# Optimization experiments

Hardware: AMD Instinct MI355X
Metric: run time of the kernel (lower is better)

## Reference

```python
import jax, jax.numpy as jnp
import numpy as np

B, C, H, W = 4, 64, 64, 64
CQ = C // 8

def setup_inputs() -> dict:
    key = jax.random.key(0)
    ks = jax.random.split(key, 8)
    s = 1.0 / np.sqrt(C)
    return {
        "x": jax.random.normal(ks[0], (B, C, H, W), dtype=jnp.float32),
        "Wq": jax.random.normal(ks[1], (CQ, C), dtype=jnp.float32) * s,
        "bq": jax.random.normal(ks[2], (CQ,), dtype=jnp.float32) * 0.01,
        "Wk": jax.random.normal(ks[3], (CQ, C), dtype=jnp.float32) * s,
        "bk": jax.random.normal(ks[4], (CQ,), dtype=jnp.float32) * 0.01,
        "Wv": jax.random.normal(ks[5], (C, C), dtype=jnp.float32) * s,
        "bv": jax.random.normal(ks[6], (C,), dtype=jnp.float32) * 0.01,
        "gamma": jax.random.normal(ks[7], (1,), dtype=jnp.float32) * 0.1,
    }

def reference(x, Wq, bq, Wk, bk, Wv, bv, gamma):
    b, c, h, w = x.shape
    n = h * w
    xf = x.reshape(b, c, n)  # [B, C, N]
    # 1x1 convs are pointwise channel projections
    q = jnp.einsum('oc,bcn->bon', Wq, xf) + bq[None, :, None]  # [B, CQ, N]
    k = jnp.einsum('oc,bcn->bon', Wk, xf) + bk[None, :, None]  # [B, CQ, N]
    v = jnp.einsum('oc,bcn->bon', Wv, xf) + bv[None, :, None]  # [B, C, N]
    energy = jnp.einsum('bcn,bcm->bnm', q, k)                  # [B, N, N]
    attn = jax.nn.softmax(energy, axis=-1)
    out = jnp.einsum('bcm,bnm->bcn', v, attn)                  # [B, C, N]
    out = out.reshape(b, c, h, w)
    return gamma[0] * out + x
```

## Files before the change

kernel.cpp:

```cpp
#include <hip/hip_runtime.h>
#include <hip/hip_bf16.h>


typedef __attribute__((ext_vector_type(8))) short short8;
typedef __attribute__((ext_vector_type(4))) float f32x4;
typedef unsigned short ushort_t;

#define NSEQ 4096
#define LOG2E 1.4426950408889634f

__device__ __forceinline__ unsigned pk_bf16(float lo, float hi) {
  union { __hip_bfloat16 b; unsigned short u; } cl, ch;
  cl.b = __float2bfloat16(lo);
  ch.b = __float2bfloat16(hi);
  return (unsigned)cl.u | ((unsigned)ch.u << 16);
}

__global__ __launch_bounds__(256, 4) void proj_kernel(
    const float* __restrict__ x,
    const float* __restrict__ Wq, const float* __restrict__ bq,
    const float* __restrict__ Wk, const float* __restrict__ bk,
    const float* __restrict__ Wv, const float* __restrict__ bv,
    ushort_t* __restrict__ Qb, ushort_t* __restrict__ Kb,
    ushort_t* __restrict__ Vb)
{
  const int tid  = threadIdx.x;
  const int lane = tid & 63;
  const int w    = __builtin_amdgcn_readfirstlane(tid >> 6);
  const int blk  = blockIdx.x;
  const int quarter = blk & 3;
  const int g    = (blk >> 2) & 63;
  const int b    = blk >> 8;
  const int n    = g * 64 + lane;

  const float* xb = x + (size_t)(b * 64) * NSEQ + n;
  const int co0 = quarter * 16 + w * 4;
  const float* w0 = Wv + (co0 + 0) * 64;
  const float* w1 = Wv + (co0 + 1) * 64;
  const float* w2 = Wv + (co0 + 2) * 64;
  const float* w3 = Wv + (co0 + 3) * 64;
  const int p = quarter * 4 + w;
  const float* wr = (p < 8) ? (Wq + p * 64) : (Wk + (p - 8) * 64);
  float a0 = bv[co0 + 0], a1 = bv[co0 + 1], a2 = bv[co0 + 2], a3 = bv[co0 + 3];
  float aq = (p < 8) ? bq[p] : bk[p - 8];

#pragma unroll
  for (int kc = 0; kc < 64; kc += 8) {
    float xv[8];
#pragma unroll
    for (int i = 0; i < 8; ++i) xv[i] = xb[(size_t)(kc + i) * NSEQ];
#pragma unroll
    for (int i = 0; i < 8; ++i) {
      const float xk = xv[i];
      a0 += w0[kc + i] * xk;
      a1 += w1[kc + i] * xk;
      a2 += w2[kc + i] * xk;
      a3 += w3[kc + i] * xk;
      aq += wr[kc + i] * xk;
    }
  }

  union { __hip_bfloat16 h; ushort_t u; } cv;
  ushort_t* vt = Vb + ((size_t)(b * 128 + (n >> 5)) * 64 + co0) * 32 + (n & 31);
  cv.h = __float2bfloat16(a0); vt[0]  = cv.u;
  cv.h = __float2bfloat16(a1); vt[32] = cv.u;
  cv.h = __float2bfloat16(a2); vt[64] = cv.u;
  cv.h = __float2bfloat16(a3); vt[96] = cv.u;

  ushort_t* qk = ((p < 8) ? Qb : Kb) + ((size_t)(b * NSEQ + n)) * 8 + (p & 7);
  cv.h = __float2bfloat16(aq); *qk = cv.u;
}

__global__ __launch_bounds__(256, 2) void attn_kernel(
    const ushort_t* __restrict__ Qb, const ushort_t* __restrict__ Kb,
    const ushort_t* __restrict__ Vb, const float* __restrict__ x,
    const float* __restrict__ gamma, float* __restrict__ out)
{
  __shared__ unsigned P_lds[2][4][2][256];
  __shared__ float red[4][64][35];

  const int tid  = threadIdx.x;
  const int wave = __builtin_amdgcn_readfirstlane(tid >> 6);
  const int lane = tid & 63;
  const int q16  = lane & 15;
  const int quad = lane >> 4;
  const int blk  = blockIdx.x;
  const int b    = blk >> 7;
  const int n0   = (blk & 127) << 5;
  const int mbase = wave << 10;

  const short8 z8 = {0, 0, 0, 0, 0, 0, 0, 0};
  short8 qfA = *(const short8*)(Qb + ((size_t)(b * NSEQ + n0 + q16)) * 8);
  short8 qfB = *(const short8*)(Qb + ((size_t)(b * NSEQ + n0 + 16 + q16)) * 8);
  if (quad != 0) { qfA = z8; qfB = z8; }

  const char* kbase = (const char*)(Kb + ((size_t)(b * NSEQ + mbase + q16)) * 8);
  const char* vbase = (const char*)(Vb + ((size_t)(b * 128 + (mbase >> 5)) * 64) * 32);
  const int voff = q16 * 64 + quad * 16;

  const int sw    = (q16 ^ (q16 >> 2)) & 3;
  const int row16 = q16 * 16;
  const int d0 = 2 * quad, d2 = 8 + 2 * quad;
  const int w00 = row16 + (((d0 >> 2) ^ sw) << 2) + (d0 & 3);
  const int w01 = row16 + ((((d0 + 1) >> 2) ^ sw) << 2) + ((d0 + 1) & 3);
  const int w10 = row16 + (((d2 >> 2) ^ sw) << 2) + (d2 & 3);
  const int w11 = row16 + ((((d2 + 1) >> 2) ^ sw) << 2) + ((d2 + 1) & 3);
  const int rdo = row16 + ((quad ^ sw) << 2);

  f32x4 aA0 = {0.f, 0.f, 0.f, 0.f};
  f32x4 aA1 = aA0, aA2 = aA0, aA3 = aA0;
  f32x4 aB0 = aA0, aB1 = aA0, aB2 = aA0, aB3 = aA0;
  float lA = 0.f, lB = 0.f;

  short8 kf0 = *(const short8*)(kbase);
  short8 kf1 = *(const short8*)(kbase + 256);
  short8 vf0 = *(const short8*)(vbase + voff);
  short8 vf1 = *(const short8*)(vbase + voff + 1024);
  short8 vf2 = *(const short8*)(vbase + voff + 2048);
  short8 vf3 = *(const short8*)(vbase + voff + 3072);

#pragma unroll 2
  for (int t = 0; t < 32; ++t) {
    const int tn = (t + 1 < 32) ? (t + 1) : 31;
    const size_t ko = (size_t)tn * 512;
    const size_t vo = (size_t)tn * 4096 + voff;
    short8 nk0 = *(const short8*)(kbase + ko);
    short8 nk1 = *(const short8*)(kbase + ko + 256);
    short8 nv0 = *(const short8*)(vbase + vo);
    short8 nv1 = *(const short8*)(vbase + vo + 1024);
    short8 nv2 = *(const short8*)(vbase + vo + 2048);
    short8 nv3 = *(const short8*)(vbase + vo + 3072);

    const f32x4 z = {0.f, 0.f, 0.f, 0.f};
    f32x4 s0 = __builtin_amdgcn_mfma_f32_16x16x32_bf16(kf0, qfA, z, 0, 0, 0);
    f32x4 s1 = __builtin_amdgcn_mfma_f32_16x16x32_bf16(kf1, qfA, z, 0, 0, 0);
    f32x4 s2 = __builtin_amdgcn_mfma_f32_16x16x32_bf16(kf0, qfB, z, 0, 0, 0);
    f32x4 s3 = __builtin_amdgcn_mfma_f32_16x16x32_bf16(kf1, qfB, z, 0, 0, 0);

    float pA0 = __builtin_amdgcn_exp2f(s0[0] * LOG2E);
    float pA1 = __builtin_amdgcn_exp2f(s0[1] * LOG2E);
    float pA2 = __builtin_amdgcn_exp2f(s0[2] * LOG2E);
    float pA3 = __builtin_amdgcn_exp2f(s0[3] * LOG2E);
    float pA4 = __builtin_amdgcn_exp2f(s1[0] * LOG2E);
    float pA5 = __builtin_amdgcn_exp2f(s1[1] * LOG2E);
    float pA6 = __builtin_amdgcn_exp2f(s1[2] * LOG2E);
    float pA7 = __builtin_amdgcn_exp2f(s1[3] * LOG2E);
    float pB0 = __builtin_amdgcn_exp2f(s2[0] * LOG2E);
    float pB1 = __builtin_amdgcn_exp2f(s2[1] * LOG2E);
    float pB2 = __builtin_amdgcn_exp2f(s2[2] * LOG2E);
    float pB3 = __builtin_amdgcn_exp2f(s2[3] * LOG2E);
    float pB4 = __builtin_amdgcn_exp2f(s3[0] * LOG2E);
    float pB5 = __builtin_amdgcn_exp2f(s3[1] * LOG2E);
    float pB6 = __builtin_amdgcn_exp2f(s3[2] * LOG2E);
    float pB7 = __builtin_amdgcn_exp2f(s3[3] * LOG2E);
    lA += ((pA0 + pA1) + (pA2 + pA3)) + ((pA4 + pA5) + (pA6 + pA7));
    lB += ((pB0 + pB1) + (pB2 + pB3)) + ((pB4 + pB5) + (pB6 + pB7));

    unsigned* pbA = &P_lds[t & 1][wave][0][0];
    unsigned* pbB = &P_lds[t & 1][wave][1][0];
    pbA[w00] = pk_bf16(pA0, pA1);
    pbA[w01] = pk_bf16(pA2, pA3);
    pbA[w10] = pk_bf16(pA4, pA5);
    pbA[w11] = pk_bf16(pA6, pA7);
    pbB[w00] = pk_bf16(pB0, pB1);
    pbB[w01] = pk_bf16(pB2, pB3);
    pbB[w10] = pk_bf16(pB4, pB5);
    pbB[w11] = pk_bf16(pB6, pB7);
    const short8 pfA = *(const short8*)(pbA + rdo);
    const short8 pfB = *(const short8*)(pbB + rdo);

    aA0 = __builtin_amdgcn_mfma_f32_16x16x32_bf16(pfA, vf0, aA0, 0, 0, 0);
    aA1 = __builtin_amdgcn_mfma_f32_16x16x32_bf16(pfA, vf1, aA1, 0, 0, 0);
    aA2 = __builtin_amdgcn_mfma_f32_16x16x32_bf16(pfA, vf2, aA2, 0, 0, 0);
    aA3 = __builtin_amdgcn_mfma_f32_16x16x32_bf16(pfA, vf3, aA3, 0, 0, 0);
    aB0 = __builtin_amdgcn_mfma_f32_16x16x32_bf16(pfB, vf0, aB0, 0, 0, 0);
    aB1 = __builtin_amdgcn_mfma_f32_16x16x32_bf16(pfB, vf1, aB1, 0, 0, 0);
    aB2 = __builtin_amdgcn_mfma_f32_16x16x32_bf16(pfB, vf2, aB2, 0, 0, 0);
    aB3 = __builtin_amdgcn_mfma_f32_16x16x32_bf16(pfB, vf3, aB3, 0, 0, 0);

    kf0 = nk0; kf1 = nk1;
    vf0 = nv0; vf1 = nv1; vf2 = nv2; vf3 = nv3;
  }

  lA += __shfl_xor(lA, 16); lA += __shfl_xor(lA, 32);
  lB += __shfl_xor(lB, 16); lB += __shfl_xor(lB, 32);

  const f32x4 aAs[4] = {aA0, aA1, aA2, aA3};
  const f32x4 aBs[4] = {aB0, aB1, aB2, aB3};
#pragma unroll
  for (int j = 0; j < 4; ++j) {
#pragma unroll
    for (int r = 0; r < 4; ++r) {
      red[wave][lane][j * 4 + r]      = aAs[j][r];
      red[wave][lane][16 + j * 4 + r] = aBs[j][r];
    }
  }
  red[wave][lane][32] = lA;
  red[wave][lane][33] = lB;
  __syncthreads();

  float frA[4] = {0.f, 0.f, 0.f, 0.f};
  float frB[4] = {0.f, 0.f, 0.f, 0.f};
  float ltA = 0.f, ltB = 0.f;
#pragma unroll
  for (int w2 = 0; w2 < 4; ++w2) {
    ltA += red[w2][lane][32];
    ltB += red[w2][lane][33];
#pragma unroll
    for (int r = 0; r < 4; ++r) {
      frA[r] += red[w2][lane][wave * 4 + r];
      frB[r] += red[w2][lane][16 + wave * 4 + r];
    }
  }

  const float g = gamma[0];
  const int c = wave * 16 + q16;
#pragma unroll
  for (int r = 0; r < 4; ++r) {
    const int rr = quad * 4 + r;
    const float lrA = __shfl(ltA, rr);
    const float lrB = __shfl(ltB, rr);
    const size_t iA = ((size_t)(b * 64 + c)) * NSEQ + n0 + rr;
    const size_t iB = iA + 16;
    out[iA] = g * (frA[r] / lrA) + x[iA];
    out[iB] = g * (frB[r] / lrB) + x[iB];
  }
}

extern "C" void kernel_launch(void* const* d_in, const int* in_sizes, int n_in,
                              void* d_out, int out_size, void* d_ws, size_t ws_size,
                              hipStream_t stream) {
  (void)in_sizes; (void)n_in; (void)out_size; (void)ws_size;
  const float* x     = (const float*)d_in[0];
  const float* Wq    = (const float*)d_in[1];
  const float* bq    = (const float*)d_in[2];
  const float* Wk    = (const float*)d_in[3];
  const float* bk    = (const float*)d_in[4];
  const float* Wv    = (const float*)d_in[5];
  const float* bv    = (const float*)d_in[6];
  const float* gamma = (const float*)d_in[7];
  float* out = (float*)d_out;

  ushort_t* Qb = (ushort_t*)d_ws;
  ushort_t* Kb = (ushort_t*)((char*)d_ws + (256u << 10));
  ushort_t* Vb = (ushort_t*)((char*)d_ws + (512u << 10));

  hipLaunchKernelGGL(proj_kernel, dim3(1024), dim3(256), 0, stream,
                     x, Wq, bq, Wk, bk, Wv, bv, Qb, Kb, Vb);
  hipLaunchKernelGGL(attn_kernel, dim3(512), dim3(256), 0, stream,
                     Qb, Kb, Vb, x, gamma, out);
}
```

Before: 99.16 us.

## Split attention key range across eight waves per block with two-stage reduction

Doubles the attention block to 512 threads, so each of eight waves handles 512 keys instead of 1024, halving the serial loop length per wave. The cross-wave reduction becomes two-stage: the upper waves write partials to shared memory and the lower waves add them in. The final reduce and store is then split across all eight waves by query half and channel group. This raises wave-level parallelism per CU to hide latency in the split-K loop, at the cost of an extra barrier, more shared memory traffic and a launch bound requiring lower register use.

```diff
diff --git a/kernel.cpp b/kernel.cpp
--- a/kernel.cpp
+++ b/kernel.cpp
@@ -71,13 +71,13 @@
   cv.h = __float2bfloat16(aq); *qk = cv.u;
 }
 
-__global__ __launch_bounds__(256, 2) void attn_kernel(
+__global__ __launch_bounds__(512, 4) void attn_kernel(
     const ushort_t* __restrict__ Qb, const ushort_t* __restrict__ Kb,
     const ushort_t* __restrict__ Vb, const float* __restrict__ x,
     const float* __restrict__ gamma, float* __restrict__ out)
 {
-  __shared__ unsigned P_lds[2][4][2][256];
-  __shared__ float red[4][64][35];
+  __shared__ unsigned P_lds[2][8][2][256];
+  __shared__ float buf[4][64][36];
 
   const int tid  = threadIdx.x;
   const int wave = __builtin_amdgcn_readfirstlane(tid >> 6);
@@ -87,7 +87,7 @@
   const int blk  = blockIdx.x;
   const int b    = blk >> 7;
   const int n0   = (blk & 127) << 5;
-  const int mbase = wave << 10;
+  const int mbase = wave << 9;
 
   const short8 z8 = {0, 0, 0, 0, 0, 0, 0, 0};
   short8 qfA = *(const short8*)(Qb + ((size_t)(b * NSEQ + n0 + q16)) * 8);
@@ -120,8 +120,8 @@
   short8 vf3 = *(const short8*)(vbase + voff + 3072);
 
 #pragma unroll 2
-  for (int t = 0; t < 32; ++t) {
-    const int tn = (t + 1 < 32) ? (t + 1) : 31;
+  for (int t = 0; t < 16; ++t) {
+    const int tn = (t + 1 < 16) ? (t + 1) : 15;
     const size_t ko = (size_t)tn * 512;
     const size_t vo = (size_t)tn * 4096 + voff;
     short8 nk0 = *(const short8*)(kbase + ko);
@@ -185,45 +185,61 @@
   lA += __shfl_xor(lA, 16); lA += __shfl_xor(lA, 32);
   lB += __shfl_xor(lB, 16); lB += __shfl_xor(lB, 32);
 
-  const f32x4 aAs[4] = {aA0, aA1, aA2, aA3};
-  const f32x4 aBs[4] = {aB0, aB1, aB2, aB3};
-#pragma unroll
-  for (int j = 0; j < 4; ++j) {
-#pragma unroll
-    for (int r = 0; r < 4; ++r) {
-      red[wave][lane][j * 4 + r]      = aAs[j][r];
-      red[wave][lane][16 + j * 4 + r] = aBs[j][r];
-    }
-  }
-  red[wave][lane][32] = lA;
-  red[wave][lane][33] = lB;
+  f32x4 aAs[4] = {aA0, aA1, aA2, aA3};
+  f32x4 aBs[4] = {aB0, aB1, aB2, aB3};
+
+  if (wave >= 4) {
+    float* d = &buf[wave - 4][lane][0];
+#pragma unroll
+    for (int j = 0; j < 4; ++j)
+#pragma unroll
+      for (int r = 0; r < 4; ++r) {
+        d[j * 4 + r]      = aAs[j][r];
+        d[16 + j * 4 + r] = aBs[j][r];
+      }
+    d[32] = lA; d[33] = lB;
+  }
   __syncthreads();
-
-  float frA[4] = {0.f, 0.f, 0.f, 0.f};
-  float frB[4] = {0.f, 0.f, 0.f, 0.f};
-  float ltA = 0.f, ltB = 0.f;
+  if (wave < 4) {
+    float* d = &buf[wave][lane][0];
+#pragma unroll
+    for (int j = 0; j < 4; ++j)
+#pragma unroll
+      for (int r = 0; r < 4; ++r) {
+        aAs[j][r] += d[j * 4 + r];
+        aBs[j][r] += d[16 + j * 4 + r];
+      }
+    lA += d[32]; lB += d[33];
+#pragma unroll
+    for (int j = 0; j < 4; ++j)
+#pragma unroll
+      for (int r = 0; r < 4; ++r) {
+        d[j * 4 + r]      = aAs[j][r];
+        d[16 + j * 4 + r] = aBs[j][r];
+      }
+    d[32] = lA; d[33] = lB;
+  }
+  __syncthreads();
+
+  const int qt = wave >> 2;
+  const int cg = wave & 3;
+  float fr[4] = {0.f, 0.f, 0.f, 0.f};
+  float lt = 0.f;
 #pragma unroll
   for (int w2 = 0; w2 < 4; ++w2) {
-    ltA += red[w2][lane][32];
-    ltB += red[w2][lane][33];
-#pragma unroll
-    for (int r = 0; r < 4; ++r) {
-      frA[r] += red[w2][lane][wave * 4 + r];
-      frB[r] += red[w2][lane][16 + wave * 4 + r];
-    }
+    lt += buf[w2][lane][32 + qt];
+#pragma unroll
+    for (int r = 0; r < 4; ++r) fr[r] += buf[w2][lane][qt * 16 + cg * 4 + r];
   }
 
   const float g = gamma[0];
-  const int c = wave * 16 + q16;
+  const int c = cg * 16 + q16;
 #pragma unroll
   for (int r = 0; r < 4; ++r) {
     const int rr = quad * 4 + r;
-    const float lrA = __shfl(ltA, rr);
-    const float lrB = __shfl(ltB, rr);
-    const size_t iA = ((size_t)(b * 64 + c)) * NSEQ + n0 + rr;
-    const size_t iB = iA + 16;
-    out[iA] = g * (frA[r] / lrA) + x[iA];
-    out[iB] = g * (frB[r] / lrB) + x[iB];
+    const float lr = __shfl(lt, rr);
+    const size_t idx = ((size_t)(b * 64 + c)) * NSEQ + n0 + qt * 16 + rr;
+    out[idx] = g * (fr[r] / lr) + x[idx];
   }
 }
 
@@ -247,6 +263,6 @@
 
   hipLaunchKernelGGL(proj_kernel, dim3(1024), dim3(256), 0, stream,
                      x, Wq, bq, Wk, bk, Wv, bv, Qb, Kb, Vb);
-  hipLaunchKernelGGL(attn_kernel, dim3(512), dim3(256), 0, stream,
+  hipLaunchKernelGGL(attn_kernel, dim3(512), dim3(512), 0, stream,
                      Qb, Kb, Vb, x, gamma, out);
 }
```

After: 97.23 us. No clear change (-1.9%).
